# Kernel optimization log

Measured on AMD Instinct MI355X. Metric: run time of the kernel, lower is better.

The kernel has to match this reference:

```python
import jax, jax.numpy as jnp
import numpy as np

DIM = 64
K = 8192
EPS = 1e-5


def setup_inputs() -> dict:
    key = jax.random.key(0)
    k1, k2, k3 = jax.random.split(key, 3)
    x = jax.random.normal(k1, (8, 4096, DIM), dtype=jnp.float32)
    mask = jnp.ones((8, 4096), dtype=bool)
    # frozen buffer: randn(K, D) * D**-0.5
    frozen_codebook = jax.random.normal(k2, (K, DIM), dtype=jnp.float32) * DIM ** -0.5
    # nn.Linear(D, D, bias=False) weight, shape (out, in) = (DIM, DIM)
    W = jax.random.normal(k3, (DIM, DIM), dtype=jnp.float32) * DIM ** -0.5
    return {"x": x, "mask": mask, "frozen_codebook": frozen_codebook, "W": W}


def reference(x, mask, frozen_codebook, W):
    # implicit codebook = Linear(frozen_codebook): [K, D]
    codebook = frozen_codebook @ W.T
    D = x.shape[-1]
    xf = x.reshape(-1, D)  # [N, D]
    mf = mask.reshape(-1)
    sq = jnp.sum(codebook * codebook, axis=-1)[None, :] - 2.0 * (xf @ codebook.T)  # [N, K]
    indices = jnp.argmin(jax.lax.stop_gradient(sq), axis=-1)  # [N]
    quantized = codebook[indices]  # embedding gather, [N, D]
    diff = quantized - xf
    dist_magnitude = jnp.linalg.norm(diff, axis=-1, keepdims=True)  # [N, 1]
    dist_magnitude = dist_magnitude * mf[:, None].astype(dist_magnitude.dtype)
    direction = diff / jnp.maximum(dist_magnitude, EPS)
    # DiVeQ trick: magnitude carries gradient, direction is detached
    quantized_out = xf + dist_magnitude * jax.lax.stop_gradient(direction)
    quantized_out = quantized_out.reshape(x.shape)
    indices = indices.reshape(x.shape[:-1])
    loss = jnp.asarray(0.0, dtype=x.dtype)
    return quantized_out, indices, loss
```

## Files before the change

### kernel.cpp

```cpp
#include <hip/hip_runtime.h>
#include <math.h>
#include <float.h>


#define DIM    64
#define KCODES 8192
#define NROWS  32768
#define EPSQ   1e-5f
#define NCHUNK 4
#define KCHUNK (KCODES / NCHUNK)
#define CTILE  128
#define LDSROW 72

typedef _Float16 half8  __attribute__((ext_vector_type(8)));
typedef float    floatx4 __attribute__((ext_vector_type(4)));

__global__ __launch_bounds__(256) void cb_prep(const float* __restrict__ frozen,
                                               const float* __restrict__ W,
                                               _Float16* __restrict__ ch,
                                               _Float16* __restrict__ cl,
                                               float* __restrict__ gh) {
    __shared__ float Wl[DIM * 65];
    __shared__ float fz[4 * DIM];
    const int tid = threadIdx.x;

    for (int i = tid; i < DIM * DIM; i += 256) {
        int d = i >> 6, j = i & 63;
        Wl[d * 65 + j] = W[i];
    }
    const int kbase = blockIdx.x * 4;
    fz[tid] = frozen[kbase * DIM + tid];
    __syncthreads();

    const int kl = tid >> 6;
    const int d  = tid & 63;
    float dot = 0.f;
#pragma unroll
    for (int j = 0; j < DIM; j++)
        dot = fmaf(fz[kl * DIM + j], Wl[d * 65 + j], dot);

    const int k = kbase + kl;
    _Float16 h = (_Float16)dot;
    ch[(size_t)k * DIM + d] = h;
    cl[(size_t)k * DIM + d] = (_Float16)(dot - (float)h);

    float s = dot * dot;
#pragma unroll
    for (int off = 32; off >= 1; off >>= 1)
        s += __shfl_xor(s, off, 64);
    if (d == 0) gh[k] = 0.5f * s;
}

__global__ __launch_bounds__(256, 4) void dist_argmin_mfma(
        const float* __restrict__ x,
        const _Float16* __restrict__ ch,
        const _Float16* __restrict__ cl,
        const float* __restrict__ gh,
        float* __restrict__ pd,
        float* __restrict__ pif) {
    __shared__ _Float16 chs[CTILE * LDSROW];
    __shared__ _Float16 cls[CTILE * LDSROW];
    __shared__ float    ghs[CTILE];
    const int tid  = threadIdx.x;
    const int wave = tid >> 6, lane = tid & 63;
    const int col  = lane & 15, quad = lane >> 4;
    const int rowblock = blockIdx.x * 128;
    const int chunk    = blockIdx.y;
    const int k0       = chunk * KCHUNK;

    half8 axh[2][2], axl[2][2];
#pragma unroll
    for (int rt = 0; rt < 2; rt++) {
        const int row = rowblock + wave * 32 + rt * 16 + col;
        const floatx4* px = (const floatx4*)(x + (size_t)row * DIM);
#pragma unroll
        for (int h = 0; h < 2; h++) {
            floatx4 f0 = px[(h * 4 + quad) * 2];
            floatx4 f1 = px[(h * 4 + quad) * 2 + 1];
            half8 hi, lo;
#pragma unroll
            for (int j = 0; j < 4; j++) {
                float v = f0[j]; _Float16 hh = (_Float16)v;
                hi[j] = hh; lo[j] = (_Float16)(v - (float)hh);
            }
#pragma unroll
            for (int j = 0; j < 4; j++) {
                float v = f1[j]; _Float16 hh = (_Float16)v;
                hi[4 + j] = hh; lo[4 + j] = (_Float16)(v - (float)hh);
            }
            axh[rt][h] = hi; axl[rt][h] = lo;
        }
    }

    float best[2][4], bidx[2][4];
#pragma unroll
    for (int rt = 0; rt < 2; rt++)
#pragma unroll
        for (int r = 0; r < 4; r++) { best[rt][r] = FLT_MAX; bidx[rt][r] = 0.f; }

    for (int t = 0; t < KCHUNK; t += CTILE) {
        __syncthreads();
        {
            const uint4* gch = (const uint4*)(ch + (size_t)(k0 + t) * DIM);
            const uint4* gcl = (const uint4*)(cl + (size_t)(k0 + t) * DIM);
#pragma unroll
            for (int i0 = 0; i0 < 1024; i0 += 256) {
                int i = i0 + tid;
                int n = i >> 3, j = i & 7;
                *(uint4*)(chs + n * LDSROW + j * 8) = gch[i];
                *(uint4*)(cls + n * LDSROW + j * 8) = gcl[i];
            }
            if (tid < CTILE) ghs[tid] = gh[k0 + t + tid];
        }
        __syncthreads();

        for (int sub = 0; sub < CTILE / 16; sub++) {
            const int n = sub * 16 + col;
            const half8 bh0 = *(const half8*)(chs + n * LDSROW + quad * 8);
            const half8 bh1 = *(const half8*)(chs + n * LDSROW + (4 + quad) * 8);
            const half8 bl0 = *(const half8*)(cls + n * LDSROW + quad * 8);
            const half8 bl1 = *(const half8*)(cls + n * LDSROW + (4 + quad) * 8);
            const float gv   = ghs[n];
            const float fidx = (float)(k0 + t + n);
#pragma unroll
            for (int rt = 0; rt < 2; rt++) {
                floatx4 acc = {0.f, 0.f, 0.f, 0.f};
                acc = __builtin_amdgcn_mfma_f32_16x16x32_f16(axh[rt][0], bh0, acc, 0, 0, 0);
                acc = __builtin_amdgcn_mfma_f32_16x16x32_f16(axh[rt][1], bh1, acc, 0, 0, 0);
                acc = __builtin_amdgcn_mfma_f32_16x16x32_f16(axl[rt][0], bh0, acc, 0, 0, 0);
                acc = __builtin_amdgcn_mfma_f32_16x16x32_f16(axl[rt][1], bh1, acc, 0, 0, 0);
                acc = __builtin_amdgcn_mfma_f32_16x16x32_f16(axh[rt][0], bl0, acc, 0, 0, 0);
                acc = __builtin_amdgcn_mfma_f32_16x16x32_f16(axh[rt][1], bl1, acc, 0, 0, 0);
#pragma unroll
                for (int r = 0; r < 4; r++) {
                    float s = gv - acc[r];
                    if (s < best[rt][r]) { best[rt][r] = s; bidx[rt][r] = fidx; }
                }
            }
        }
    }

#pragma unroll
    for (int rt = 0; rt < 2; rt++)
#pragma unroll
        for (int r = 0; r < 4; r++) {
            float v = best[rt][r], ix = bidx[rt][r];
#pragma unroll
            for (int off = 8; off >= 1; off >>= 1) {
                float v2 = __shfl_xor(v, off, 16);
                float i2 = __shfl_xor(ix, off, 16);
                if (v2 < v || (v2 == v && i2 < ix)) { v = v2; ix = i2; }
            }
            if (col == 0) {
                const int row = rowblock + wave * 32 + rt * 16 + quad * 4 + r;
                pd [(size_t)chunk * NROWS + row] = v;
                pif[(size_t)chunk * NROWS + row] = ix;
            }
        }
}

__global__ __launch_bounds__(256) void finalize(const float* __restrict__ x,
                                                const _Float16* __restrict__ ch,
                                                const _Float16* __restrict__ cl,
                                                const float* __restrict__ pd,
                                                const float* __restrict__ pif,
                                                float* __restrict__ out) {
    const int row = blockIdx.x * 256 + threadIdx.x;

    float best = pd[row];
    float bix  = pif[row];
#pragma unroll
    for (int c = 1; c < NCHUNK; c++) {
        float d2 = pd[(size_t)c * NROWS + row];
        float i2 = pif[(size_t)c * NROWS + row];
        if (d2 < best) { best = d2; bix = i2; }
    }
    const int bidx = (int)bix;

    const half8*  qh = (const half8*)(ch + (size_t)bidx * DIM);
    const half8*  ql = (const half8*)(cl + (size_t)bidx * DIM);
    const floatx4* xp = (const floatx4*)(x + (size_t)row * DIM);
    float diff[DIM], xr[DIM], ss = 0.f;
#pragma unroll
    for (int i = 0; i < 8; i++) {
        half8 hh = qh[i], ll = ql[i];
#pragma unroll
        for (int j = 0; j < 8; j++) {
            float c = (float)hh[j] + (float)ll[j];
            int d = i * 8 + j;
            xr[d] = x[(size_t)row * DIM + d];
            diff[d] = c - xr[d];
        }
    }
#pragma unroll
    for (int d = 0; d < DIM; d++) ss = fmaf(diff[d], diff[d], ss);

    const float dist = sqrtf(ss);
    const float dm   = fmaxf(dist, EPSQ);
    floatx4* op = (floatx4*)(out + (size_t)row * DIM);
#pragma unroll
    for (int i = 0; i < DIM / 4; i++) {
        floatx4 o;
#pragma unroll
        for (int j = 0; j < 4; j++)
            o[j] = fmaf(dist, diff[i * 4 + j] / dm, xr[i * 4 + j]);
        op[i] = o;
    }
    out[(size_t)NROWS * DIM + row] = (float)bidx;
    if (row == 0) out[(size_t)NROWS * DIM + NROWS] = 0.f;
    (void)xp;
}

extern "C" void kernel_launch(void* const* d_in, const int* in_sizes, int n_in,
                              void* d_out, int out_size, void* d_ws, size_t ws_size,
                              hipStream_t stream) {
    const float* x      = (const float*)d_in[0];
    const float* frozen = (const float*)d_in[2];
    const float* W      = (const float*)d_in[3];
    float* out = (float*)d_out;

    char* ws = (char*)d_ws;
    _Float16* ch = (_Float16*)ws;
    _Float16* cl = ch + (size_t)KCODES * DIM;
    float*    gh = (float*)(ws + 2u * KCODES * DIM * sizeof(_Float16));
    float*    pd = gh + KCODES;
    float*    pif = pd + (size_t)NCHUNK * NROWS;

    cb_prep<<<KCODES / 4, 256, 0, stream>>>(frozen, W, ch, cl, gh);
    dist_argmin_mfma<<<dim3(NROWS / 128, NCHUNK), 256, 0, stream>>>(x, ch, cl, gh, pd, pif);
    finalize<<<NROWS / 256, 256, 0, stream>>>(x, ch, cl, pd, pif, out);
}
```

Measured before the change: 189.2 us.

## Pre-swizzle codebook into MFMA fragment layout, load via global_load_lds, widen row tiles

```diff
diff --git a/kernel.cpp b/kernel.cpp
--- a/kernel.cpp
+++ b/kernel.cpp
@@ -7,18 +7,30 @@
 #define KCODES 8192
 #define NROWS  32768
 #define EPSQ   1e-5f
-#define NCHUNK 4
+#define NCHUNK 8
 #define KCHUNK (KCODES / NCHUNK)
 #define CTILE  128
-#define LDSROW 72
-
-typedef _Float16 half8  __attribute__((ext_vector_type(8)));
+
+typedef _Float16 half8   __attribute__((ext_vector_type(8)));
 typedef float    floatx4 __attribute__((ext_vector_type(4)));
+
+typedef const void __attribute__((address_space(1))) gvoid;
+typedef void       __attribute__((address_space(3))) lvoid;
+
+__device__ __forceinline__ void load_lds16(const void* g, void* l) {
+#if __has_builtin(__builtin_amdgcn_global_load_lds)
+    __builtin_amdgcn_global_load_lds((gvoid*)g, (lvoid*)l, 16, 0, 0);
+#else
+    int lane = threadIdx.x & 63;
+    *(uint4*)((char*)l + lane * 16) = *(const uint4*)((const char*)g + lane * 16);
+#endif
+}
+
 
 __global__ __launch_bounds__(256) void cb_prep(const float* __restrict__ frozen,
                                                const float* __restrict__ W,
-                                               _Float16* __restrict__ ch,
-                                               _Float16* __restrict__ cl,
+                                               _Float16* __restrict__ chg,
+                                               _Float16* __restrict__ clg,
                                                float* __restrict__ gh) {
     __shared__ float Wl[DIM * 65];
     __shared__ float fz[4 * DIM];
@@ -40,38 +52,40 @@
         dot = fmaf(fz[kl * DIM + j], Wl[d * 65 + j], dot);
 
     const int k = kbase + kl;
+    const int s = k >> 4, col = k & 15, j = d >> 3, e = d & 7;
+    const size_t off = ((size_t)(s * 8 + j) * 16 + col) * 8 + e;
     _Float16 h = (_Float16)dot;
-    ch[(size_t)k * DIM + d] = h;
-    cl[(size_t)k * DIM + d] = (_Float16)(dot - (float)h);
-
-    float s = dot * dot;
-#pragma unroll
-    for (int off = 32; off >= 1; off >>= 1)
-        s += __shfl_xor(s, off, 64);
-    if (d == 0) gh[k] = 0.5f * s;
-}
-
-__global__ __launch_bounds__(256, 4) void dist_argmin_mfma(
+    chg[off] = h;
+    clg[off] = (_Float16)(dot - (float)h);
+
+    float ssum = dot * dot;
+#pragma unroll
+    for (int offx = 32; offx >= 1; offx >>= 1)
+        ssum += __shfl_xor(ssum, offx, 64);
+    if (d == 0) gh[k] = 0.5f * ssum;
+}
+
+__global__ __launch_bounds__(256, 3) void dist_argmin_mfma(
         const float* __restrict__ x,
-        const _Float16* __restrict__ ch,
-        const _Float16* __restrict__ cl,
+        const _Float16* __restrict__ chg,
+        const _Float16* __restrict__ clg,
         const float* __restrict__ gh,
         float* __restrict__ pd,
         float* __restrict__ pif) {
-    __shared__ _Float16 chs[CTILE * LDSROW];
-    __shared__ _Float16 cls[CTILE * LDSROW];
+    __shared__ _Float16 chs[CTILE * DIM];
+    __shared__ _Float16 cls[CTILE * DIM];
     __shared__ float    ghs[CTILE];
     const int tid  = threadIdx.x;
     const int wave = tid >> 6, lane = tid & 63;
     const int col  = lane & 15, quad = lane >> 4;
-    const int rowblock = blockIdx.x * 128;
+    const int rowblock = blockIdx.x * 256;
     const int chunk    = blockIdx.y;
     const int k0       = chunk * KCHUNK;
 
-    half8 axh[2][2], axl[2][2];
-#pragma unroll
-    for (int rt = 0; rt < 2; rt++) {
-        const int row = rowblock + wave * 32 + rt * 16 + col;
+    half8 axh[4][2], axl[4][2];
+#pragma unroll
+    for (int rt = 0; rt < 4; rt++) {
+        const int row = rowblock + wave * 64 + rt * 16 + col;
         const floatx4* px = (const floatx4*)(x + (size_t)row * DIM);
 #pragma unroll
         for (int h = 0; h < 2; h++) {
@@ -79,51 +93,50 @@
             floatx4 f1 = px[(h * 4 + quad) * 2 + 1];
             half8 hi, lo;
 #pragma unroll
-            for (int j = 0; j < 4; j++) {
-                float v = f0[j]; _Float16 hh = (_Float16)v;
-                hi[j] = hh; lo[j] = (_Float16)(v - (float)hh);
-            }
-#pragma unroll
-            for (int j = 0; j < 4; j++) {
-                float v = f1[j]; _Float16 hh = (_Float16)v;
-                hi[4 + j] = hh; lo[4 + j] = (_Float16)(v - (float)hh);
+            for (int jj = 0; jj < 4; jj++) {
+                float v = f0[jj]; _Float16 hh = (_Float16)v;
+                hi[jj] = hh; lo[jj] = (_Float16)(v - (float)hh);
+            }
+#pragma unroll
+            for (int jj = 0; jj < 4; jj++) {
+                float v = f1[jj]; _Float16 hh = (_Float16)v;
+                hi[4 + jj] = hh; lo[4 + jj] = (_Float16)(v - (float)hh);
             }
             axh[rt][h] = hi; axl[rt][h] = lo;
         }
     }
 
-    float best[2][4], bidx[2][4];
-#pragma unroll
-    for (int rt = 0; rt < 2; rt++)
+    float best[4][4], bidx[4][4];
+#pragma unroll
+    for (int rt = 0; rt < 4; rt++)
 #pragma unroll
         for (int r = 0; r < 4; r++) { best[rt][r] = FLT_MAX; bidx[rt][r] = 0.f; }
 
     for (int t = 0; t < KCHUNK; t += CTILE) {
         __syncthreads();
         {
-            const uint4* gch = (const uint4*)(ch + (size_t)(k0 + t) * DIM);
-            const uint4* gcl = (const uint4*)(cl + (size_t)(k0 + t) * DIM);
-#pragma unroll
-            for (int i0 = 0; i0 < 1024; i0 += 256) {
-                int i = i0 + tid;
-                int n = i >> 3, j = i & 7;
-                *(uint4*)(chs + n * LDSROW + j * 8) = gch[i];
-                *(uint4*)(cls + n * LDSROW + j * 8) = gcl[i];
+            const _Float16* gch = chg + (size_t)(k0 + t) * DIM;
+            const _Float16* gcl = clg + (size_t)(k0 + t) * DIM;
+#pragma unroll
+            for (int i = 0; i < 4; i++) {
+                const int seg = i * 4 + wave;
+                load_lds16(gch + seg * 512 + lane * 8, (char*)chs + seg * 1024);
+                load_lds16(gcl + seg * 512 + lane * 8, (char*)cls + seg * 1024);
             }
             if (tid < CTILE) ghs[tid] = gh[k0 + t + tid];
         }
         __syncthreads();
 
+#pragma unroll 2
         for (int sub = 0; sub < CTILE / 16; sub++) {
-            const int n = sub * 16 + col;
-            const half8 bh0 = *(const half8*)(chs + n * LDSROW + quad * 8);
-            const half8 bh1 = *(const half8*)(chs + n * LDSROW + (4 + quad) * 8);
-            const half8 bl0 = *(const half8*)(cls + n * LDSROW + quad * 8);
-            const half8 bl1 = *(const half8*)(cls + n * LDSROW + (4 + quad) * 8);
-            const float gv   = ghs[n];
-            const float fidx = (float)(k0 + t + n);
-#pragma unroll
-            for (int rt = 0; rt < 2; rt++) {
+            const half8 bh0 = *(const half8*)(chs + sub * 1024 +       lane * 8);
+            const half8 bh1 = *(const half8*)(chs + sub * 1024 + 512 + lane * 8);
+            const half8 bl0 = *(const half8*)(cls + sub * 1024 +       lane * 8);
+            const half8 bl1 = *(const half8*)(cls + sub * 1024 + 512 + lane * 8);
+            const float gv   = ghs[sub * 16 + col];
+            const float fidx = (float)(k0 + t + sub * 16 + col);
+#pragma unroll
+            for (int rt = 0; rt < 4; rt++) {
                 floatx4 acc = {0.f, 0.f, 0.f, 0.f};
                 acc = __builtin_amdgcn_mfma_f32_16x16x32_f16(axh[rt][0], bh0, acc, 0, 0, 0);
                 acc = __builtin_amdgcn_mfma_f32_16x16x32_f16(axh[rt][1], bh1, acc, 0, 0, 0);
@@ -133,15 +146,15 @@
                 acc = __builtin_amdgcn_mfma_f32_16x16x32_f16(axh[rt][1], bl1, acc, 0, 0, 0);
 #pragma unroll
                 for (int r = 0; r < 4; r++) {
-                    float s = gv - acc[r];
-                    if (s < best[rt][r]) { best[rt][r] = s; bidx[rt][r] = fidx; }
+                    float sc = gv - acc[r];
+                    if (sc < best[rt][r]) { best[rt][r] = sc; bidx[rt][r] = fidx; }
                 }
             }
         }
     }
 
 #pragma unroll
-    for (int rt = 0; rt < 2; rt++)
+    for (int rt = 0; rt < 4; rt++)
 #pragma unroll
         for (int r = 0; r < 4; r++) {
             float v = best[rt][r], ix = bidx[rt][r];
@@ -152,7 +165,7 @@
                 if (v2 < v || (v2 == v && i2 < ix)) { v = v2; ix = i2; }
             }
             if (col == 0) {
-                const int row = rowblock + wave * 32 + rt * 16 + quad * 4 + r;
+                const int row = rowblock + wave * 64 + rt * 16 + quad * 4 + r;
                 pd [(size_t)chunk * NROWS + row] = v;
                 pif[(size_t)chunk * NROWS + row] = ix;
             }
@@ -160,8 +173,8 @@
 }
 
 __global__ __launch_bounds__(256) void finalize(const float* __restrict__ x,
-                                                const _Float16* __restrict__ ch,
-                                                const _Float16* __restrict__ cl,
+                                                const _Float16* __restrict__ chg,
+                                                const _Float16* __restrict__ clg,
                                                 const float* __restrict__ pd,
                                                 const float* __restrict__ pif,
                                                 float* __restrict__ out) {
@@ -177,17 +190,17 @@
     }
     const int bidx = (int)bix;
 
-    const half8*  qh = (const half8*)(ch + (size_t)bidx * DIM);
-    const half8*  ql = (const half8*)(cl + (size_t)bidx * DIM);
-    const floatx4* xp = (const floatx4*)(x + (size_t)row * DIM);
+    const int s = bidx >> 4, cc = bidx & 15;
     float diff[DIM], xr[DIM], ss = 0.f;
 #pragma unroll
-    for (int i = 0; i < 8; i++) {
-        half8 hh = qh[i], ll = ql[i];
-#pragma unroll
-        for (int j = 0; j < 8; j++) {
-            float c = (float)hh[j] + (float)ll[j];
-            int d = i * 8 + j;
+    for (int j = 0; j < 8; j++) {
+        const size_t off = ((size_t)(s * 8 + j) * 16 + cc) * 8;
+        half8 hh = *(const half8*)(chg + off);
+        half8 ll = *(const half8*)(clg + off);
+#pragma unroll
+        for (int e = 0; e < 8; e++) {
+            const int d = j * 8 + e;
+            float c = (float)hh[e] + (float)ll[e];
             xr[d] = x[(size_t)row * DIM + d];
             diff[d] = c - xr[d];
         }
@@ -202,13 +215,12 @@
     for (int i = 0; i < DIM / 4; i++) {
         floatx4 o;
 #pragma unroll
-        for (int j = 0; j < 4; j++)
-            o[j] = fmaf(dist, diff[i * 4 + j] / dm, xr[i * 4 + j]);
+        for (int jj = 0; jj < 4; jj++)
+            o[jj] = fmaf(dist, diff[i * 4 + jj] / dm, xr[i * 4 + jj]);
         op[i] = o;
     }
     out[(size_t)NROWS * DIM + row] = (float)bidx;
     if (row == 0) out[(size_t)NROWS * DIM + NROWS] = 0.f;
-    (void)xp;
 }
 
 extern "C" void kernel_launch(void* const* d_in, const int* in_sizes, int n_in,
@@ -220,13 +232,13 @@
     float* out = (float*)d_out;
 
     char* ws = (char*)d_ws;
-    _Float16* ch = (_Float16*)ws;
-    _Float16* cl = ch + (size_t)KCODES * DIM;
-    float*    gh = (float*)(ws + 2u * KCODES * DIM * sizeof(_Float16));
-    float*    pd = gh + KCODES;
+    _Float16* chg = (_Float16*)ws;
+    _Float16* clg = chg + (size_t)KCODES * DIM;
+    float*    gh  = (float*)(ws + 2u * KCODES * DIM * sizeof(_Float16));
+    float*    pd  = gh + KCODES;
     float*    pif = pd + (size_t)NCHUNK * NROWS;
 
-    cb_prep<<<KCODES / 4, 256, 0, stream>>>(frozen, W, ch, cl, gh);
-    dist_argmin_mfma<<<dim3(NROWS / 128, NCHUNK), 256, 0, stream>>>(x, ch, cl, gh, pd, pif);
-    finalize<<<NROWS / 256, 256, 0, stream>>>(x, ch, cl, pd, pif, out);
-}
+    cb_prep<<<KCODES / 4, 256, 0, stream>>>(frozen, W, chg, clg, gh);
+    dist_argmin_mfma<<<dim3(NROWS / 256, NCHUNK), 256, 0, stream>>>(x, chg, clg, gh, pd, pif);
+    finalize<<<NROWS / 256, 256, 0, stream>>>(x, chg, clg, pd, pif, out);
+}
```

Result: faster. 179.4 us (-5.2%).
